# Performance work log

Hardware: AMD Instinct MI355X
Metric: run time of the kernel (lower is better)

Reference implementation:

```python
import jax, jax.numpy as jnp
import numpy as np

H = 28
W = 28
CIN = 128
COUT = 32
K = 3
SHIFT = 1  # fixed shift_direction (original draws +/-1 at init)


def setup_inputs() -> dict:
    key = jax.random.key(0)
    kx, kw = jax.random.split(key)
    x = jax.random.normal(kx, (512, CIN, H, W), dtype=jnp.float32)
    w = jax.random.normal(kw, (COUT, CIN, K), dtype=jnp.float32)
    return {"x": x, "w": w}


def reference(x, w):
    # Original: reshape to (B, C*H, W, 1), unfold with kernel (3,1) pad (1,0)
    # -> conv with kernel 3 along the W axis, then einsum contracts channel
    # and kernel dims (128->32), then roll by +1 along H.
    B = x.shape[0]
    xp = jnp.pad(x, ((0, 0), (0, 0), (0, 0), (1, 1)))  # pad W by 1 each side
    # windows: (B, CIN, H, K, W) — mirrors the unfold+reshape to (1,128,28,3,28)
    win = jnp.stack([xp[..., k:k + W] for k in range(K)], axis=3)
    # einsum 'limkn, jik -> ljmn' with batch dim: contract channel i and tap k
    y = jnp.einsum('bihkn,jik->bjhn', win, w)  # (B, COUT, H, W)
    # permute->(B,H,COUT,W), roll along H, permute back == roll on axis 2 here
    y = jnp.roll(y, SHIFT, axis=2)
    return y
```

## Files before the change

kernel.cpp:

```cpp
#include <hip/hip_runtime.h>

#define CIN_  128
#define H_    28
#define W_    28
#define COUT_ 32
#define B_    512

typedef __attribute__((ext_vector_type(8))) short short8;
typedef __attribute__((ext_vector_type(4))) float f32x4;

__device__ __forceinline__ short f2bf(float f) {
    union { float f; unsigned u; } v; v.f = f;
    unsigned u = v.u + 0x7fffu + ((v.u >> 16) & 1u);
    return (short)(u >> 16);
}

__global__ void prep_w_kernel(const float* __restrict__ w, short* __restrict__ wsA) {
    int t = blockIdx.x * 256 + threadIdx.x;
    int frag = t >> 9;
    int rem  = t & 511;
    int l = rem >> 3;
    int j = rem & 7;
    int mt = frag / 12;
    int kc = frag % 12;
    int tap = kc >> 2;
    int i  = (kc & 3) * 32 + (l >> 4) * 8 + j;
    int jo = mt * 16 + (l & 15);
    wsA[t] = f2bf(w[(jo * CIN_ + i) * 3 + tap]);
}

template<bool USE_WS>
__global__ __launch_bounds__(128, 5)
void conv_kernel(const float* __restrict__ x, const float* __restrict__ w,
                 const short* __restrict__ wsA, float* __restrict__ out) {
    __shared__ short lds[2][34 * CIN_];
    const int tid = threadIdx.x;
    const int wv  = tid >> 6;
    const int l   = tid & 63;
    const int hg  = blockIdx.x;
    const int b   = blockIdx.y;
    const int h0  = hg * 2;

    const float* xb = x + (size_t)b * (CIN_ * H_ * W_);

    {
        int e   = tid * 4;
        int buf = e >> 8;
        int row = ((e >> 7) & 1) ? 29 : 0;
        int c   = e & 127;
        *reinterpret_cast<ulong1*>(&lds[buf][row * CIN_ + c]) = ulong1{0};
    }

#pragma unroll
    for (int t = 0; t < 14; ++t) {
        int f4  = t * 128 + tid;
        int i   = f4 / 14;
        int rem = f4 % 14;
        int hl  = rem / 7;
        int w4  = rem % 7;
        f32x4 v = *reinterpret_cast<const f32x4*>(xb + i * (H_ * W_) + (h0 + hl) * W_ + w4 * 4);
        short* buf = lds[hl];
#pragma unroll
        for (int e = 0; e < 4; ++e) {
            int wt   = w4 * 4 + e + 1;
            int sidx = wt * CIN_ + ((((i >> 3) ^ (wt & 15)) << 3) | (i & 7));
            buf[sidx] = f2bf(v[e]);
        }
    }
    __syncthreads();

    short* wbuf = lds[wv];
    const int h = h0 + wv;

    f32x4 acc[2][2];
#pragma unroll
    for (int mt = 0; mt < 2; ++mt)
#pragma unroll
        for (int nt = 0; nt < 2; ++nt)
#pragma unroll
            for (int q = 0; q < 4; ++q) acc[mt][nt][q] = 0.0f;

#pragma unroll
    for (int half = 0; half < 2; ++half) {
        short8 a0[6], a1[6];
        if (USE_WS) {
#pragma unroll
            for (int k6 = 0; k6 < 6; ++k6) {
                int kc = half * 6 + k6;
                a0[k6] = *reinterpret_cast<const short8*>(wsA + kc * 512 + l * 8);
                a1[k6] = *reinterpret_cast<const short8*>(wsA + (12 + kc) * 512 + l * 8);
            }
        } else {
#pragma unroll
            for (int k6 = 0; k6 < 6; ++k6) {
                int kc  = half * 6 + k6;
                int tap = kc >> 2;
                int ib  = (kc & 3) * 32 + (l >> 4) * 8;
#pragma unroll
                for (int j = 0; j < 8; ++j) {
                    a0[k6][j] = f2bf(w[((l & 15) * CIN_ + ib + j) * 3 + tap]);
                    a1[k6][j] = f2bf(w[((16 + (l & 15)) * CIN_ + ib + j) * 3 + tap]);
                }
            }
        }
#pragma unroll
        for (int k6 = 0; k6 < 6; ++k6) {
            int kc  = half * 6 + k6;
            int tap = kc >> 2;
            int c   = (kc & 3) * 4 + (l >> 4);
#pragma unroll
            for (int nt = 0; nt < 2; ++nt) {
                int wt = nt * 16 + (l & 15) + tap;
                const short8 bfrag = *reinterpret_cast<const short8*>(
                    &wbuf[wt * CIN_ + ((c ^ (wt & 15)) << 3)]);
                acc[0][nt] = __builtin_amdgcn_mfma_f32_16x16x32_bf16(
                    a0[k6], bfrag, acc[0][nt], 0, 0, 0);
                acc[1][nt] = __builtin_amdgcn_mfma_f32_16x16x32_bf16(
                    a1[k6], bfrag, acc[1][nt], 0, 0, 0);
            }
        }
    }

    float* ob = out + (size_t)b * (COUT_ * H_ * W_);
    const int ho = (h + 1 == H_) ? 0 : (h + 1);
#pragma unroll
    for (int mt = 0; mt < 2; ++mt)
#pragma unroll
        for (int nt = 0; nt < 2; ++nt)
#pragma unroll
            for (int rr = 0; rr < 4; ++rr) {
                int j    = mt * 16 + (l >> 4) * 4 + rr;
                int wcol = nt * 16 + (l & 15);
                if (wcol < W_)
                    ob[(j * H_ + ho) * W_ + wcol] = acc[mt][nt][rr];
            }
}

extern "C" void kernel_launch(void* const* d_in, const int* in_sizes, int n_in,
                              void* d_out, int out_size, void* d_ws, size_t ws_size,
                              hipStream_t stream) {
    (void)in_sizes; (void)n_in; (void)out_size;
    const float* x = (const float*)d_in[0];
    const float* w = (const float*)d_in[1];
    float* out = (float*)d_out;

    if (ws_size >= (size_t)(24 * 512 * sizeof(short))) {
        short* wsA = (short*)d_ws;
        prep_w_kernel<<<dim3(48), dim3(256), 0, stream>>>(w, wsA);
        conv_kernel<true><<<dim3(14, 512), dim3(128), 0, stream>>>(x, w, wsA, out);
    } else {
        conv_kernel<false><<<dim3(14, 512), dim3(128), 0, stream>>>(x, w, (const short*)nullptr, out);
    }
}
```

Measured before the change: 69.88 us.

## Use single-wave blocks per output row, drop block barrier, prefetch weights early

Each block now handles one H row with a single 64-lane wavefront instead of two rows with two waves. This removes the __syncthreads in favour of an lgkmcnt wait and issues the first half of the weight fragments before staging x into LDS so their latency overlaps. Global loads are batched seven at a time ahead of the bf16 conversion, out-of-range window rows are clamped to the zero-padded row, and the float-to-bf16 conversion now uses the HIP intrinsic. The grid doubles and LDS per block halves, which raises block count and occupancy potential but adds per-block overhead and weight reloads.

```diff
diff --git a/kernel.cpp b/kernel.cpp
--- a/kernel.cpp
+++ b/kernel.cpp
@@ -1,4 +1,5 @@
 #include <hip/hip_runtime.h>
+#include <hip/hip_bf16.h>
 
 #define CIN_  128
 #define H_    28
@@ -10,9 +11,9 @@
 typedef __attribute__((ext_vector_type(4))) float f32x4;
 
 __device__ __forceinline__ short f2bf(float f) {
-    union { float f; unsigned u; } v; v.f = f;
-    unsigned u = v.u + 0x7fffu + ((v.u >> 16) & 1u);
-    return (short)(u >> 16);
+    __hip_bfloat16 h = __float2bfloat16(f);
+    union { __hip_bfloat16 h; short s; } u; u.h = h;
+    return u.s;
 }
 
 __global__ void prep_w_kernel(const float* __restrict__ w, short* __restrict__ wsA) {
@@ -30,47 +31,65 @@
 }
 
 template<bool USE_WS>
-__global__ __launch_bounds__(128, 5)
+__global__ __launch_bounds__(64, 5)
 void conv_kernel(const float* __restrict__ x, const float* __restrict__ w,
                  const short* __restrict__ wsA, float* __restrict__ out) {
-    __shared__ short lds[2][34 * CIN_];
-    const int tid = threadIdx.x;
-    const int wv  = tid >> 6;
-    const int l   = tid & 63;
-    const int hg  = blockIdx.x;
-    const int b   = blockIdx.y;
-    const int h0  = hg * 2;
+    __shared__ short wbuf[30 * CIN_];
+    const int l = threadIdx.x;
+    const int h = blockIdx.x;
+    const int b = blockIdx.y;
 
     const float* xb = x + (size_t)b * (CIN_ * H_ * W_);
 
-    {
-        int e   = tid * 4;
-        int buf = e >> 8;
-        int row = ((e >> 7) & 1) ? 29 : 0;
-        int c   = e & 127;
-        *reinterpret_cast<ulong1*>(&lds[buf][row * CIN_ + c]) = ulong1{0};
+    *reinterpret_cast<int*>(&wbuf[0 * CIN_ + l * 2])  = 0;
+    *reinterpret_cast<int*>(&wbuf[29 * CIN_ + l * 2]) = 0;
+
+    short8 a0[6], a1[6];
+    if (USE_WS) {
+#pragma unroll
+        for (int k6 = 0; k6 < 6; ++k6) {
+            a0[k6] = *reinterpret_cast<const short8*>(wsA + k6 * 512 + l * 8);
+            a1[k6] = *reinterpret_cast<const short8*>(wsA + (12 + k6) * 512 + l * 8);
+        }
+    } else {
+#pragma unroll
+        for (int k6 = 0; k6 < 6; ++k6) {
+            int tap = k6 >> 2;
+            int ib  = (k6 & 3) * 32 + (l >> 4) * 8;
+#pragma unroll
+            for (int j = 0; j < 8; ++j) {
+                a0[k6][j] = f2bf(w[((l & 15) * CIN_ + ib + j) * 3 + tap]);
+                a1[k6][j] = f2bf(w[((16 + (l & 15)) * CIN_ + ib + j) * 3 + tap]);
+            }
+        }
     }
 
 #pragma unroll
-    for (int t = 0; t < 14; ++t) {
-        int f4  = t * 128 + tid;
-        int i   = f4 / 14;
-        int rem = f4 % 14;
-        int hl  = rem / 7;
-        int w4  = rem % 7;
-        f32x4 v = *reinterpret_cast<const f32x4*>(xb + i * (H_ * W_) + (h0 + hl) * W_ + w4 * 4);
-        short* buf = lds[hl];
+    for (int half = 0; half < 2; ++half) {
+        f32x4 vb[7];
 #pragma unroll
-        for (int e = 0; e < 4; ++e) {
-            int wt   = w4 * 4 + e + 1;
-            int sidx = wt * CIN_ + ((((i >> 3) ^ (wt & 15)) << 3) | (i & 7));
-            buf[sidx] = f2bf(v[e]);
+        for (int it = 0; it < 7; ++it) {
+            int f4 = (half * 7 + it) * 64 + l;
+            int i  = f4 / 7;
+            int w4 = f4 % 7;
+            vb[it] = *reinterpret_cast<const f32x4*>(xb + i * (H_ * W_) + h * W_ + w4 * 4);
+        }
+#pragma unroll
+        for (int it = 0; it < 7; ++it) {
+            int f4 = (half * 7 + it) * 64 + l;
+            int i  = f4 / 7;
+            int w4 = f4 % 7;
+#pragma unroll
+            for (int e = 0; e < 4; ++e) {
+                int wt   = w4 * 4 + e + 1;
+                int sidx = wt * CIN_ + ((((i >> 3) ^ (wt & 15)) << 3) | (i & 7));
+                wbuf[sidx] = f2bf(vb[it][e]);
+            }
         }
     }
-    __syncthreads();
 
-    short* wbuf = lds[wv];
-    const int h = h0 + wv;
+    asm volatile("s_waitcnt lgkmcnt(0)" ::: "memory");
+    __builtin_amdgcn_sched_barrier(0);
 
     f32x4 acc[2][2];
 #pragma unroll
@@ -82,24 +101,25 @@
 
 #pragma unroll
     for (int half = 0; half < 2; ++half) {
-        short8 a0[6], a1[6];
-        if (USE_WS) {
+        if (half == 1) {
+            if (USE_WS) {
 #pragma unroll
-            for (int k6 = 0; k6 < 6; ++k6) {
-                int kc = half * 6 + k6;
-                a0[k6] = *reinterpret_cast<const short8*>(wsA + kc * 512 + l * 8);
-                a1[k6] = *reinterpret_cast<const short8*>(wsA + (12 + kc) * 512 + l * 8);
-            }
-        } else {
+                for (int k6 = 0; k6 < 6; ++k6) {
+                    int kc = 6 + k6;
+                    a0[k6] = *reinterpret_cast<const short8*>(wsA + kc * 512 + l * 8);
+                    a1[k6] = *reinterpret_cast<const short8*>(wsA + (12 + kc) * 512 + l * 8);
+                }
+            } else {
 #pragma unroll
-            for (int k6 = 0; k6 < 6; ++k6) {
-                int kc  = half * 6 + k6;
-                int tap = kc >> 2;
-                int ib  = (kc & 3) * 32 + (l >> 4) * 8;
+                for (int k6 = 0; k6 < 6; ++k6) {
+                    int kc  = 6 + k6;
+                    int tap = kc >> 2;
+                    int ib  = (kc & 3) * 32 + (l >> 4) * 8;
 #pragma unroll
-                for (int j = 0; j < 8; ++j) {
-                    a0[k6][j] = f2bf(w[((l & 15) * CIN_ + ib + j) * 3 + tap]);
-                    a1[k6][j] = f2bf(w[((16 + (l & 15)) * CIN_ + ib + j) * 3 + tap]);
+                    for (int j = 0; j < 8; ++j) {
+                        a0[k6][j] = f2bf(w[((l & 15) * CIN_ + ib + j) * 3 + tap]);
+                        a1[k6][j] = f2bf(w[((16 + (l & 15)) * CIN_ + ib + j) * 3 + tap]);
+                    }
                 }
             }
         }
@@ -110,9 +130,10 @@
             int c   = (kc & 3) * 4 + (l >> 4);
 #pragma unroll
             for (int nt = 0; nt < 2; ++nt) {
-                int wt = nt * 16 + (l & 15) + tap;
+                int wt  = nt * 16 + (l & 15) + tap;
+                int wtc = wt > 29 ? 29 : wt;
                 const short8 bfrag = *reinterpret_cast<const short8*>(
-                    &wbuf[wt * CIN_ + ((c ^ (wt & 15)) << 3)]);
+                    &wbuf[wtc * CIN_ + ((c ^ (wtc & 15)) << 3)]);
                 acc[0][nt] = __builtin_amdgcn_mfma_f32_16x16x32_bf16(
                     a0[k6], bfrag, acc[0][nt], 0, 0, 0);
                 acc[1][nt] = __builtin_amdgcn_mfma_f32_16x16x32_bf16(
@@ -147,8 +168,8 @@
     if (ws_size >= (size_t)(24 * 512 * sizeof(short))) {
         short* wsA = (short*)d_ws;
         prep_w_kernel<<<dim3(48), dim3(256), 0, stream>>>(w, wsA);
-        conv_kernel<true><<<dim3(14, 512), dim3(128), 0, stream>>>(x, w, wsA, out);
+        conv_kernel<true><<<dim3(28, 512), dim3(64), 0, stream>>>(x, w, wsA, out);
     } else {
-        conv_kernel<false><<<dim3(14, 512), dim3(128), 0, stream>>>(x, w, (const short*)nullptr, out);
+        conv_kernel<false><<<dim3(28, 512), dim3(64), 0, stream>>>(x, w, (const short*)nullptr, out);
     }
 }
```

Result: slower. 96.61 us (+38.2%).

## Process four rows per block with 256 threads and batched global loads

Applied to the files above, without the earlier changes.

Each block now handles four output rows with four waves instead of two rows with two waves. The grid shrinks from 14 to 7 blocks per image, and the per-row LDS buffers shrink from 34 to 30 rows, with out-of-range tap reads clamped to row 29. The staging loop now issues seven 16-byte global loads into registers before converting and writing them to LDS, which aims for more loads in flight and contiguous 112-byte row segments per channel. The bf16 conversion switches to the HIP intrinsic, and the larger blocks raise register and LDS pressure per block, which may reduce occupancy.

```diff
diff --git a/kernel.cpp b/kernel.cpp
--- a/kernel.cpp
+++ b/kernel.cpp
@@ -1,4 +1,5 @@
 #include <hip/hip_runtime.h>
+#include <hip/hip_bf16.h>
 
 #define CIN_  128
 #define H_    28
@@ -10,9 +11,9 @@
 typedef __attribute__((ext_vector_type(4))) float f32x4;
 
 __device__ __forceinline__ short f2bf(float f) {
-    union { float f; unsigned u; } v; v.f = f;
-    unsigned u = v.u + 0x7fffu + ((v.u >> 16) & 1u);
-    return (short)(u >> 16);
+    __hip_bfloat16 h = __float2bfloat16(f);
+    union { __hip_bfloat16 h; short s; } u; u.h = h;
+    return u.s;
 }
 
 __global__ void prep_w_kernel(const float* __restrict__ w, short* __restrict__ wsA) {
@@ -30,41 +31,50 @@
 }
 
 template<bool USE_WS>
-__global__ __launch_bounds__(128, 5)
+__global__ __launch_bounds__(256, 5)
 void conv_kernel(const float* __restrict__ x, const float* __restrict__ w,
                  const short* __restrict__ wsA, float* __restrict__ out) {
-    __shared__ short lds[2][34 * CIN_];
+    __shared__ short lds[4][30 * CIN_];
     const int tid = threadIdx.x;
     const int wv  = tid >> 6;
     const int l   = tid & 63;
     const int hg  = blockIdx.x;
     const int b   = blockIdx.y;
-    const int h0  = hg * 2;
+    const int h0  = hg * 4;
 
     const float* xb = x + (size_t)b * (CIN_ * H_ * W_);
 
     {
-        int e   = tid * 4;
-        int buf = e >> 8;
-        int row = ((e >> 7) & 1) ? 29 : 0;
-        int c   = e & 127;
-        *reinterpret_cast<ulong1*>(&lds[buf][row * CIN_ + c]) = ulong1{0};
+        int s   = (tid & 63) * 4;
+        int row = (s >= 128) ? 29 : 0;
+        int c   = s & 127;
+        *reinterpret_cast<ulong1*>(&lds[wv][row * CIN_ + c]) = ulong1{0};
     }
 
 #pragma unroll
-    for (int t = 0; t < 14; ++t) {
-        int f4  = t * 128 + tid;
-        int i   = f4 / 14;
-        int rem = f4 % 14;
-        int hl  = rem / 7;
-        int w4  = rem % 7;
-        f32x4 v = *reinterpret_cast<const f32x4*>(xb + i * (H_ * W_) + (h0 + hl) * W_ + w4 * 4);
-        short* buf = lds[hl];
+    for (int half = 0; half < 2; ++half) {
+        f32x4 vb[7];
 #pragma unroll
-        for (int e = 0; e < 4; ++e) {
-            int wt   = w4 * 4 + e + 1;
-            int sidx = wt * CIN_ + ((((i >> 3) ^ (wt & 15)) << 3) | (i & 7));
-            buf[sidx] = f2bf(v[e]);
+        for (int it = 0; it < 7; ++it) {
+            int f4 = (half * 7 + it) * 256 + tid;
+            int i  = f4 / 28;
+            int q  = f4 % 28;
+            vb[it] = *reinterpret_cast<const f32x4*>(xb + i * (H_ * W_) + h0 * W_ + q * 4);
+        }
+#pragma unroll
+        for (int it = 0; it < 7; ++it) {
+            int f4 = (half * 7 + it) * 256 + tid;
+            int i  = f4 / 28;
+            int q  = f4 % 28;
+            int hl = q / 7;
+            int w4 = q % 7;
+            short* buf = lds[hl];
+#pragma unroll
+            for (int e = 0; e < 4; ++e) {
+                int wt   = w4 * 4 + e + 1;
+                int sidx = wt * CIN_ + ((((i >> 3) ^ (wt & 15)) << 3) | (i & 7));
+                buf[sidx] = f2bf(vb[it][e]);
+            }
         }
     }
     __syncthreads();
@@ -110,9 +120,10 @@
             int c   = (kc & 3) * 4 + (l >> 4);
 #pragma unroll
             for (int nt = 0; nt < 2; ++nt) {
-                int wt = nt * 16 + (l & 15) + tap;
+                int wt  = nt * 16 + (l & 15) + tap;
+                int wtc = wt > 29 ? 29 : wt;
                 const short8 bfrag = *reinterpret_cast<const short8*>(
-                    &wbuf[wt * CIN_ + ((c ^ (wt & 15)) << 3)]);
+                    &wbuf[wtc * CIN_ + ((c ^ (wtc & 15)) << 3)]);
                 acc[0][nt] = __builtin_amdgcn_mfma_f32_16x16x32_bf16(
                     a0[k6], bfrag, acc[0][nt], 0, 0, 0);
                 acc[1][nt] = __builtin_amdgcn_mfma_f32_16x16x32_bf16(
@@ -147,8 +158,8 @@
     if (ws_size >= (size_t)(24 * 512 * sizeof(short))) {
         short* wsA = (short*)d_ws;
         prep_w_kernel<<<dim3(48), dim3(256), 0, stream>>>(w, wsA);
-        conv_kernel<true><<<dim3(14, 512), dim3(128), 0, stream>>>(x, w, wsA, out);
+        conv_kernel<true><<<dim3(7, 512), dim3(256), 0, stream>>>(x, w, wsA, out);
     } else {
-        conv_kernel<false><<<dim3(14, 512), dim3(128), 0, stream>>>(x, w, (const short*)nullptr, out);
+        conv_kernel<false><<<dim3(7, 512), dim3(256), 0, stream>>>(x, w, (const short*)nullptr, out);
     }
 }
```

Measured after the change: 58.69 us. 16.0% less time.
